# Kernel optimization log

Measured on AMD Instinct MI355X. Metric: run time of the kernel, lower is better.

The kernel has to match this reference:

```python
import jax, jax.numpy as jnp
import numpy as np

# tree structure: B trees, layer sizes per tree 2048 -> 256 -> 32 -> 1 (arities 8, 8, 32)
B = 256
N0, N1, N2, N3 = B * 2048, B * 256, B * 32, B * 1
D_IN, HID, OUT = 128, 256, 10
EPS = 1e-5


def _bn(x, g, b):
    # BatchNorm1d, training-mode batch stats (biased variance), as in torch
    mu = jnp.mean(x, axis=0)
    var = jnp.var(x, axis=0)
    return (x - mu) * jax.lax.rsqrt(var + EPS) * g + b


def _tree_layer(pooled, w1, b1, bn1g, bn1b, w2, b2, bng, bnb):
    # MLP(2 layers): Linear -> BN -> ReLU -> Linear, then outer BN -> ReLU (next_layer)
    z = jax.nn.relu(_bn(pooled @ w1 + b1, bn1g, bn1b))
    z = z @ w2 + b2
    return jax.nn.relu(_bn(z, bng, bnb))


def setup_inputs() -> dict:
    key = jax.random.key(0)
    ks = jax.random.split(key, 12)
    s = 0.05
    ar = lambda n: jnp.arange(n, dtype=jnp.int32)
    inp = {
        'x': jax.random.normal(ks[0], (N0, D_IN), jnp.float32),
        # child -> parent index (global, trees are contiguous blocks)
        'parent1': ar(N0) // 8,
        'parent2': ar(N1) // 8,
        'parent3': ar(N2) // 32,
        # node -> tree id per layer (for sum tree-pooling readout)
        'tree0': ar(N0) // 2048,
        'tree1': ar(N1) // 256,
        'tree2': ar(N2) // 32,
        # layer 1 MLP (input_dim -> hidden)
        'l1_w1': jax.random.normal(ks[1], (D_IN, HID), jnp.float32) * s,
        'l1_b1': jnp.zeros((HID,), jnp.float32),
        'l1_bn1g': jnp.ones((HID,), jnp.float32),
        'l1_bn1b': jnp.zeros((HID,), jnp.float32),
        'l1_w2': jax.random.normal(ks[2], (HID, HID), jnp.float32) * s,
        'l1_b2': jnp.zeros((HID,), jnp.float32),
        'l1_bng': jnp.ones((HID,), jnp.float32),
        'l1_bnb': jnp.zeros((HID,), jnp.float32),
        # layers 2 and 3 MLPs (hidden -> hidden), stacked on axis 0
        'lw1': jax.random.normal(ks[3], (2, HID, HID), jnp.float32) * s,
        'lb1': jnp.zeros((2, HID), jnp.float32),
        'lbn1g': jnp.ones((2, HID), jnp.float32),
        'lbn1b': jnp.zeros((2, HID), jnp.float32),
        'lw2': jax.random.normal(ks[4], (2, HID, HID), jnp.float32) * s,
        'lb2': jnp.zeros((2, HID), jnp.float32),
        'lbng': jnp.ones((2, HID), jnp.float32),
        'lbnb': jnp.zeros((2, HID), jnp.float32),
        # prediction heads
        'pred0_w': jax.random.normal(ks[5], (D_IN, OUT), jnp.float32) * s,
        'pred0_b': jnp.zeros((OUT,), jnp.float32),
        'predh_w': jax.random.normal(ks[6], (3, HID, OUT), jnp.float32) * s,
        'predh_b': jnp.zeros((3, OUT), jnp.float32),
    }
    return inp


def reference(x, parent1, parent2, parent3, tree0, tree1, tree2,
              l1_w1, l1_b1, l1_bn1g, l1_bn1b, l1_w2, l1_b2, l1_bng, l1_bnb,
              lw1, lb1, lbn1g, lbn1b, lw2, lb2, lbng, lbnb,
              pred0_w, pred0_b, predh_w, predh_b):
    seg = jax.ops.segment_sum
    h0 = x
    # layer 1: sparse child pooling (spmm == segment_sum) + MLP + BN + ReLU
    h1 = _tree_layer(seg(h0, parent1, num_segments=N1),
                     l1_w1, l1_b1, l1_bn1g, l1_bn1b, l1_w2, l1_b2, l1_bng, l1_bnb)
    h2 = _tree_layer(seg(h1, parent2, num_segments=N2),
                     lw1[0], lb1[0], lbn1g[0], lbn1b[0], lw2[0], lb2[0], lbng[0], lbnb[0])
    h3 = _tree_layer(seg(h2, parent3, num_segments=N3),
                     lw1[1], lb1[1], lbn1g[1], lbn1b[1], lw2[1], lb2[1], lbng[1], lbnb[1])
    # sum tree-pooling readout over layers 0..depth-1, plus root-layer linear
    score = seg(h0, tree0, num_segments=B) @ pred0_w + pred0_b
    score = score + seg(h1, tree1, num_segments=B) @ predh_w[0] + predh_b[0]
    score = score + seg(h2, tree2, num_segments=B) @ predh_w[1] + predh_b[1]
    score = score + h3 @ predh_w[2] + predh_b[2]  # h3 has 1 root per tree -> [B, OUT]
    return score
```

## Files before the change

### kernel.cpp

```cpp
#include <hip/hip_runtime.h>
#include <hip/hip_bf16.h>


#define N0 (256*2048)
#define N1 (256*256)
#define N2 (256*32)
#define NB 256
#define BN_EPS 1e-5f
#define NSLOT 8

typedef __attribute__((ext_vector_type(8))) __bf16 bf16x8;
typedef __attribute__((ext_vector_type(8))) unsigned short u16x8;
typedef __attribute__((ext_vector_type(4))) unsigned short u16x4;
typedef __attribute__((ext_vector_type(4))) float f32x4;

__device__ inline float bf2f(unsigned short b) {
    unsigned u = ((unsigned)b) << 16;
    float f; __builtin_memcpy(&f, &u, 4); return f;
}
__device__ inline unsigned short f2bf(float f) {
    unsigned u; __builtin_memcpy(&u, &f, 4);
    u += 0x7fff + ((u >> 16) & 1);
    return (unsigned short)(u >> 16);
}

__global__ __launch_bounds__(256) void prep_weights(const float* __restrict__ l1_w1,
                                                    const float* __restrict__ l1_w2,
                                                    const float* __restrict__ lw1,
                                                    const float* __restrict__ lw2,
                                                    unsigned short* __restrict__ Wt) {
    int idx = blockIdx.x * 256 + threadIdx.x;
    if (idx >= 360448) return;
    float v;
    if (idx < 32768) {
        int n = idx >> 7, k = idx & 127;
        v = l1_w1[k * 256 + n];
    } else if (idx < 98304) {
        int j = idx - 32768, n = j >> 8, k = j & 255;
        v = l1_w2[k * 256 + n];
    } else if (idx < 163840) {
        int j = idx - 98304, n = j >> 8, k = j & 255;
        v = lw1[k * 256 + n];
    } else if (idx < 229376) {
        int j = idx - 163840, n = j >> 8, k = j & 255;
        v = lw2[k * 256 + n];
    } else if (idx < 294912) {
        int j = idx - 229376, n = j >> 8, k = j & 255;
        v = lw1[65536 + k * 256 + n];
    } else {
        int j = idx - 294912, n = j >> 8, k = j & 255;
        v = lw2[65536 + k * 256 + n];
    }
    Wt[idx] = f2bf(v);
}

__device__ inline void bn_prologue(int tid, const float* __restrict__ partials,
                                   const float* __restrict__ g, const float* __restrict__ b,
                                   float invM, float* sc_lds, float* sh_lds) {
    if (tid < 256) {
        float s = 0.f, s2 = 0.f;
#pragma unroll
        for (int k = 0; k < NSLOT; ++k) {
            s  += partials[k * 512 + tid];
            s2 += partials[k * 512 + 256 + tid];
        }
        float mean = s * invM;
        float var = s2 * invM - mean * mean;
        float sc = g[tid] * rsqrtf(var + BN_EPS);
        sc_lds[tid] = sc;
        sh_lds[tid] = b[tid] - mean * sc;
    }
}

__global__ __launch_bounds__(256) void pool8_128(const float* __restrict__ x,
                                                 unsigned short* __restrict__ out,
                                                 float* __restrict__ ts0) {
    int tid = threadIdx.x;
    int c4 = tid & 31, pl = tid >> 5;
    int p = blockIdx.x * 8 + pl;
    int tree = blockIdx.x >> 5;
    const f32x4* xp = reinterpret_cast<const f32x4*>(x + (size_t)p * 8 * 128 + c4 * 4);
    f32x4 s = {0.f, 0.f, 0.f, 0.f};
#pragma unroll
    for (int c = 0; c < 8; ++c) s += xp[c * 32];
    u16x4 o;
#pragma unroll
    for (int e = 0; e < 4; ++e) o[e] = f2bf(s[e]);
    *reinterpret_cast<u16x4*>(out + (size_t)p * 128 + c4 * 4) = o;
    __shared__ float red[4][32][4];
    int w = tid >> 6;
    f32x4 t = s;
#pragma unroll
    for (int e = 0; e < 4; ++e) t[e] += __shfl_xor(t[e], 32);
    if ((tid & 63) < 32) {
#pragma unroll
        for (int e = 0; e < 4; ++e) red[w][c4][e] = t[e];
    }
    __syncthreads();
    if (tid < 128) {
        int cc = tid >> 2, e = tid & 3;
        float v = red[0][cc][e] + red[1][cc][e] + red[2][cc][e] + red[3][cc][e];
        atomicAdd(&ts0[tree * 128 + tid], v);
    }
}

template <int GROUP, bool TS>
__global__ __launch_bounds__(256) void pool_bn_relu(const unsigned short* __restrict__ Z,
                                                    const float* __restrict__ partials,
                                                    const float* __restrict__ g,
                                                    const float* __restrict__ b,
                                                    float invM,
                                                    unsigned short* __restrict__ out,
                                                    float* __restrict__ ts) {
    __shared__ float sc_lds[256], sh_lds[256];
    int tid = threadIdx.x;
    bn_prologue(tid, partials, g, b, invM, sc_lds, sh_lds);
    __syncthreads();
    int c8 = tid & 31, pl = tid >> 5;
    size_t p = (size_t)blockIdx.x * 8 + pl;
    int d0 = c8 * 8;
    float sc[8], sh[8], s[8];
#pragma unroll
    for (int e = 0; e < 8; ++e) { sc[e] = sc_lds[d0 + e]; sh[e] = sh_lds[d0 + e]; s[e] = 0.f; }
#pragma unroll
    for (int gi = 0; gi < GROUP; ++gi) {
        u16x8 z = *reinterpret_cast<const u16x8*>(Z + (p * GROUP + gi) * 256 + d0);
#pragma unroll
        for (int e = 0; e < 8; ++e) {
            float f = sc[e] * bf2f(z[e]) + sh[e];
            s[e] += f > 0.f ? f : 0.f;
        }
    }
    u16x8 o;
#pragma unroll
    for (int e = 0; e < 8; ++e) o[e] = f2bf(s[e]);
    *reinterpret_cast<u16x8*>(out + p * 256 + d0) = o;
    if (TS) {
        __shared__ float red[4][32][8];
        int tree = blockIdx.x >> 2;
        int w = tid >> 6;
#pragma unroll
        for (int e = 0; e < 8; ++e) s[e] += __shfl_xor(s[e], 32);
        if ((tid & 63) < 32) {
#pragma unroll
            for (int e = 0; e < 8; ++e) red[w][c8][e] = s[e];
        }
        __syncthreads();
        {
            int cc = tid >> 3, e = tid & 7;
            float v = red[0][cc][e] + red[1][cc][e] + red[2][cc][e] + red[3][cc][e];
            atomicAdd(&ts[tree * 256 + tid], v);
        }
    }
}

template <int KD, bool BN_A, int BM>
__global__ __launch_bounds__(BM * 4) void mfma_gemm(const unsigned short* __restrict__ A,
                                                    const float* __restrict__ partials_in,
                                                    const float* __restrict__ bn_g,
                                                    const float* __restrict__ bn_b,
                                                    float invM,
                                                    const unsigned short* __restrict__ Wt,
                                                    const float* __restrict__ bias,
                                                    unsigned short* __restrict__ C,
                                                    float* __restrict__ stat_partials) {
    constexpr int LDA = 72;
    constexpr int NT = BM * 4;
    __shared__ unsigned short Asb[BM * LDA];
    __shared__ unsigned short Bsb[256 * LDA];
    __shared__ float sc_lds[256], sh_lds[256];
    const int tid = threadIdx.x;
    if (BN_A) {
        bn_prologue(tid, partials_in, bn_g, bn_b, invM, sc_lds, sh_lds);
        __syncthreads();
    }
    const int m0 = blockIdx.x * BM;
    const int wave = tid >> 6, lane = tid & 63;
    const int q = lane >> 4, r = lane & 15;
    const int wc = wave & 3, wr = wave >> 2;

    f32x4 acc[4][4];
#pragma unroll
    for (int i = 0; i < 4; ++i)
#pragma unroll
        for (int j = 0; j < 4; ++j) acc[i][j] = (f32x4){0.f, 0.f, 0.f, 0.f};

    for (int k0 = 0; k0 < KD; k0 += 64) {
#pragma unroll
        for (int i = 0; i < 2; ++i) {
            int v = tid + i * NT;
            int row = v >> 3, kc = v & 7;
            u16x8 d = *reinterpret_cast<const u16x8*>(A + (size_t)(m0 + row) * KD + k0 + kc * 8);
            if (BN_A) {
                u16x8 o;
#pragma unroll
                for (int e = 0; e < 8; ++e) {
                    int k = k0 + kc * 8 + e;
                    float f = sc_lds[k] * bf2f(d[e]) + sh_lds[k];
                    o[e] = f2bf(f > 0.f ? f : 0.f);
                }
                d = o;
            }
            *reinterpret_cast<u16x8*>(&Asb[row * LDA + kc * 8]) = d;
        }
#pragma unroll
        for (int i = 0; i < 2048 / NT; ++i) {
            int v = tid + i * NT;
            int n = v >> 3, kc = v & 7;
            u16x8 d = *reinterpret_cast<const u16x8*>(Wt + (size_t)n * KD + k0 + kc * 8);
            *reinterpret_cast<u16x8*>(&Bsb[n * LDA + kc * 8]) = d;
        }
        __syncthreads();
#pragma unroll
        for (int s = 0; s < 2; ++s) {
            bf16x8 a[4], b[4];
#pragma unroll
            for (int i = 0; i < 4; ++i)
                a[i] = *reinterpret_cast<const bf16x8*>(&Asb[(wr * 64 + i * 16 + r) * LDA + s * 32 + q * 8]);
#pragma unroll
            for (int j = 0; j < 4; ++j)
                b[j] = *reinterpret_cast<const bf16x8*>(&Bsb[(wc * 64 + j * 16 + r) * LDA + s * 32 + q * 8]);
#pragma unroll
            for (int i = 0; i < 4; ++i)
#pragma unroll
                for (int j = 0; j < 4; ++j)
                    acc[i][j] = __builtin_amdgcn_mfma_f32_16x16x32_bf16(a[i], b[j], acc[i][j], 0, 0, 0);
        }
        __syncthreads();
    }

    float sj[4], s2j[4];
#pragma unroll
    for (int j = 0; j < 4; ++j) {
        float bj = bias[wc * 64 + j * 16 + r];
        float s = 0.f, s2 = 0.f;
#pragma unroll
        for (int i = 0; i < 4; ++i)
#pragma unroll
            for (int e = 0; e < 4; ++e) {
                acc[i][j][e] += bj;
                float v = acc[i][j][e];
                s += v; s2 += v * v;
            }
        s  += __shfl_xor(s, 16);  s  += __shfl_xor(s, 32);
        s2 += __shfl_xor(s2, 16); s2 += __shfl_xor(s2, 32);
        sj[j] = s; s2j[j] = s2;
    }
#pragma unroll
    for (int i = 0; i < 4; ++i)
#pragma unroll
        for (int e = 0; e < 4; ++e) {
            size_t row = m0 + wr * 64 + i * 16 + q * 4 + e;
#pragma unroll
            for (int j = 0; j < 4; ++j)
                C[row * 256 + wc * 64 + j * 16 + r] = f2bf(acc[i][j][e]);
        }
    if (q == 0) {
        int slot = blockIdx.x & (NSLOT - 1);
#pragma unroll
        for (int j = 0; j < 4; ++j) {
            int col = wc * 64 + j * 16 + r;
            atomicAdd(&stat_partials[slot * 512 + col], sj[j]);
            atomicAdd(&stat_partials[slot * 512 + 256 + col], s2j[j]);
        }
    }
}

__global__ __launch_bounds__(256) void head_kernel(const float* __restrict__ ts0,
                                                   const float* __restrict__ ts1,
                                                   const unsigned short* __restrict__ p3,
                                                   const unsigned short* __restrict__ Z3b,
                                                   const float* __restrict__ partials,
                                                   const float* __restrict__ g,
                                                   const float* __restrict__ b,
                                                   float invM,
                                                   const float* __restrict__ p0w,
                                                   const float* __restrict__ p0b,
                                                   const float* __restrict__ phw,
                                                   const float* __restrict__ phb,
                                                   float* __restrict__ out) {
    __shared__ float sc_lds[256], sh_lds[256];
    int t = blockIdx.x, d = threadIdx.x;
    bn_prologue(d, partials, g, b, invM, sc_lds, sh_lds);
    __syncthreads();
    float acc[10];
#pragma unroll
    for (int o = 0; o < 10; ++o) acc[o] = 0.f;
    if (d < 128) {
        float v = ts0[t * 128 + d];
#pragma unroll
        for (int o = 0; o < 10; ++o) acc[o] += v * p0w[d * 10 + o];
    }
    {
        float v = ts1[t * 256 + d];
#pragma unroll
        for (int o = 0; o < 10; ++o) acc[o] += v * phw[d * 10 + o];
    }
    {
        float v = bf2f(p3[t * 256 + d]);
#pragma unroll
        for (int o = 0; o < 10; ++o) acc[o] += v * phw[2560 + d * 10 + o];
    }
    {
        float v = sc_lds[d] * bf2f(Z3b[t * 256 + d]) + sh_lds[d];
        v = v > 0.f ? v : 0.f;
#pragma unroll
        for (int o = 0; o < 10; ++o) acc[o] += v * phw[5120 + d * 10 + o];
    }
    __shared__ float red[256];
    for (int o = 0; o < 10; ++o) {
        red[d] = acc[o];
        __syncthreads();
        for (int s = 128; s > 0; s >>= 1) {
            if (d < s) red[d] += red[d + s];
            __syncthreads();
        }
        if (d == 0) out[t * 10 + o] = red[0] + p0b[o] + phb[o] + phb[10 + o] + phb[20 + o];
        __syncthreads();
    }
}

extern "C" void kernel_launch(void* const* d_in, const int* in_sizes, int n_in,
                              void* d_out, int out_size, void* d_ws, size_t ws_size,
                              hipStream_t stream) {
    const float* x       = (const float*)d_in[0];
    const float* l1_w1   = (const float*)d_in[7];
    const float* l1_b1   = (const float*)d_in[8];
    const float* l1_bn1g = (const float*)d_in[9];
    const float* l1_bn1b = (const float*)d_in[10];
    const float* l1_w2   = (const float*)d_in[11];
    const float* l1_b2   = (const float*)d_in[12];
    const float* l1_bng  = (const float*)d_in[13];
    const float* l1_bnb  = (const float*)d_in[14];
    const float* lw1     = (const float*)d_in[15];
    const float* lb1     = (const float*)d_in[16];
    const float* lbn1g   = (const float*)d_in[17];
    const float* lbn1b   = (const float*)d_in[18];
    const float* lw2     = (const float*)d_in[19];
    const float* lb2     = (const float*)d_in[20];
    const float* lbng    = (const float*)d_in[21];
    const float* lbnb    = (const float*)d_in[22];
    const float* pred0_w = (const float*)d_in[23];
    const float* pred0_b = (const float*)d_in[24];
    const float* predh_w = (const float*)d_in[25];
    const float* predh_b = (const float*)d_in[26];
    float* out = (float*)d_out;

    uint8_t* wsb = (uint8_t*)d_ws;
    unsigned short* pooled1 = (unsigned short*)(wsb);
    unsigned short* Z1      = (unsigned short*)(wsb + (16ull << 20));
    unsigned short* Z2      = (unsigned short*)(wsb + (48ull << 20));
    unsigned short* pooled2 = (unsigned short*)(wsb + (80ull << 20));
    unsigned short* Z2a     = (unsigned short*)(wsb + (84ull << 20));
    unsigned short* Z2b     = (unsigned short*)(wsb + (88ull << 20));
    unsigned short* pooled3 = (unsigned short*)(wsb + (92ull << 20));
    unsigned short* Z3a     = (unsigned short*)(wsb + (92ull << 20) + 131072);
    unsigned short* Z3b     = (unsigned short*)(wsb + (92ull << 20) + 262144);
    unsigned short* Wt      = (unsigned short*)(wsb + (93ull << 20));
    float* zbase = (float*)(wsb + (94ull << 20));
    float* ts0   = zbase;
    float* ts1   = zbase + 32768;
    float* stats = zbase + 32768 + 65536;
    auto SP = [&](int i) { return stats + i * (NSLOT * 512); };
    size_t zbytes = (32768 + 65536 + 6 * NSLOT * 512) * sizeof(float);

    hipMemsetAsync(zbase, 0, zbytes, stream);
    prep_weights<<<1408, 256, 0, stream>>>(l1_w1, l1_w2, lw1, lw2, Wt);

    pool8_128<<<N1 / 8, 256, 0, stream>>>(x, pooled1, ts0);
    mfma_gemm<128, false, 128><<<N1 / 128, 512, 0, stream>>>(
        pooled1, nullptr, nullptr, nullptr, 0.f, Wt, l1_b1, Z1, SP(0));
    mfma_gemm<256, true, 128><<<N1 / 128, 512, 0, stream>>>(
        Z1, SP(0), l1_bn1g, l1_bn1b, 1.f / N1, Wt + 32768, l1_b2, Z2, SP(1));
    pool_bn_relu<8, true><<<N2 / 8, 256, 0, stream>>>(
        Z2, SP(1), l1_bng, l1_bnb, 1.f / N1, pooled2, ts1);

    mfma_gemm<256, false, 64><<<N2 / 64, 256, 0, stream>>>(
        pooled2, nullptr, nullptr, nullptr, 0.f, Wt + 98304, lb1, Z2a, SP(2));
    mfma_gemm<256, true, 64><<<N2 / 64, 256, 0, stream>>>(
        Z2a, SP(2), lbn1g, lbn1b, 1.f / N2, Wt + 163840, lb2, Z2b, SP(3));
    pool_bn_relu<32, false><<<NB / 8, 256, 0, stream>>>(
        Z2b, SP(3), lbng, lbnb, 1.f / N2, pooled3, nullptr);

    mfma_gemm<256, false, 64><<<NB / 64, 256, 0, stream>>>(
        pooled3, nullptr, nullptr, nullptr, 0.f, Wt + 229376, lb1 + 256, Z3a, SP(4));
    mfma_gemm<256, true, 64><<<NB / 64, 256, 0, stream>>>(
        Z3a, SP(4), lbn1g + 256, lbn1b + 256, 1.f / NB, Wt + 294912, lb2 + 256, Z3b, SP(5));

    head_kernel<<<NB, 256, 0, stream>>>(ts0, ts1, pooled3, Z3b, SP(5),
                                        lbng + 256, lbnb + 256, 1.f / NB,
                                        pred0_w, pred0_b, predh_w, predh_b, out);
}
```

Measured before the change: 196.9 us.

## Fuse child pooling into the following GEMMs for layers one and two

The pooling of x (sum of 8 children) now happens inside the first GEMM kernel, which writes pooled rows straight to LDS instead of a global buffer. Likewise the BN+ReLU+pool of Z2 is folded into the layer-2 first GEMM, with the tree-sum readout atomics done in the same pass. This removes two kernel launches and the global write/read of pooled1 and pooled2. In exchange, each GEMM block does more serial load work before its MFMAs, the per-thread tree-sum atomics are less reduced (more atomics), and LDS use grows.

```diff
diff --git a/kernel.cpp b/kernel.cpp
--- a/kernel.cpp
+++ b/kernel.cpp
@@ -72,84 +72,225 @@
     }
 }
 
-__global__ __launch_bounds__(256) void pool8_128(const float* __restrict__ x,
-                                                 unsigned short* __restrict__ out,
-                                                 float* __restrict__ ts0) {
-    int tid = threadIdx.x;
-    int c4 = tid & 31, pl = tid >> 5;
-    int p = blockIdx.x * 8 + pl;
-    int tree = blockIdx.x >> 5;
-    const f32x4* xp = reinterpret_cast<const f32x4*>(x + (size_t)p * 8 * 128 + c4 * 4);
-    f32x4 s = {0.f, 0.f, 0.f, 0.f};
-#pragma unroll
-    for (int c = 0; c < 8; ++c) s += xp[c * 32];
-    u16x4 o;
-#pragma unroll
-    for (int e = 0; e < 4; ++e) o[e] = f2bf(s[e]);
-    *reinterpret_cast<u16x4*>(out + (size_t)p * 128 + c4 * 4) = o;
-    __shared__ float red[4][32][4];
-    int w = tid >> 6;
-    f32x4 t = s;
-#pragma unroll
-    for (int e = 0; e < 4; ++e) t[e] += __shfl_xor(t[e], 32);
-    if ((tid & 63) < 32) {
-#pragma unroll
-        for (int e = 0; e < 4; ++e) red[w][c4][e] = t[e];
-    }
+__global__ __launch_bounds__(512) void gemm1_fused(const float* __restrict__ x,
+                                                   const unsigned short* __restrict__ Wt,
+                                                   const float* __restrict__ bias,
+                                                   unsigned short* __restrict__ Z1,
+                                                   float* __restrict__ stat_partials,
+                                                   float* __restrict__ ts0) {
+    constexpr int LDA = 136, LDB = 72;
+    __shared__ unsigned short Asb[128 * LDA];
+    __shared__ unsigned short Bsb[256 * LDB];
+    const int tid = threadIdx.x;
+    const int c4 = tid & 31, rg = tid >> 5;
+    const int m0 = blockIdx.x * 128;
+    const int tree = blockIdx.x >> 1;
+    f32x4 colp = {0.f, 0.f, 0.f, 0.f};
+#pragma unroll
+    for (int i = 0; i < 8; ++i) {
+        int row = rg * 8 + i;
+        const f32x4* xp = reinterpret_cast<const f32x4*>(x + (size_t)(m0 + row) * 1024 + c4 * 4);
+        f32x4 s = {0.f, 0.f, 0.f, 0.f};
+#pragma unroll
+        for (int c = 0; c < 8; ++c) s += xp[c * 32];
+        u16x4 o;
+#pragma unroll
+        for (int e = 0; e < 4; ++e) o[e] = f2bf(s[e]);
+        *reinterpret_cast<u16x4*>(&Asb[row * LDA + c4 * 4]) = o;
+        colp += s;
+    }
+#pragma unroll
+    for (int e = 0; e < 4; ++e) atomicAdd(&ts0[tree * 128 + c4 * 4 + e], colp[e]);
+
+    const int wave = tid >> 6, lane = tid & 63;
+    const int q = lane >> 4, r = lane & 15;
+    const int wc = wave & 3, wr = wave >> 2;
+    f32x4 acc[4][4];
+#pragma unroll
+    for (int i = 0; i < 4; ++i)
+#pragma unroll
+        for (int j = 0; j < 4; ++j) acc[i][j] = (f32x4){0.f, 0.f, 0.f, 0.f};
+
+#pragma unroll
+    for (int s2 = 0; s2 < 2; ++s2) {
+#pragma unroll
+        for (int i = 0; i < 4; ++i) {
+            int v = tid + i * 512;
+            int n = v >> 3, kc = v & 7;
+            u16x8 d = *reinterpret_cast<const u16x8*>(Wt + (size_t)n * 128 + s2 * 64 + kc * 8);
+            *reinterpret_cast<u16x8*>(&Bsb[n * LDB + kc * 8]) = d;
+        }
+        __syncthreads();
+#pragma unroll
+        for (int s = 0; s < 2; ++s) {
+            bf16x8 a[4], b[4];
+#pragma unroll
+            for (int i = 0; i < 4; ++i)
+                a[i] = *reinterpret_cast<const bf16x8*>(&Asb[(wr * 64 + i * 16 + r) * LDA + s2 * 64 + s * 32 + q * 8]);
+#pragma unroll
+            for (int j = 0; j < 4; ++j)
+                b[j] = *reinterpret_cast<const bf16x8*>(&Bsb[(wc * 64 + j * 16 + r) * LDB + s * 32 + q * 8]);
+#pragma unroll
+            for (int i = 0; i < 4; ++i)
+#pragma unroll
+                for (int j = 0; j < 4; ++j)
+                    acc[i][j] = __builtin_amdgcn_mfma_f32_16x16x32_bf16(a[i], b[j], acc[i][j], 0, 0, 0);
+        }
+        __syncthreads();
+    }
+    float sj[4], s2j[4];
+#pragma unroll
+    for (int j = 0; j < 4; ++j) {
+        float bj = bias[wc * 64 + j * 16 + r];
+        float s = 0.f, s2 = 0.f;
+#pragma unroll
+        for (int i = 0; i < 4; ++i)
+#pragma unroll
+            for (int e = 0; e < 4; ++e) {
+                acc[i][j][e] += bj;
+                float v = acc[i][j][e];
+                s += v; s2 += v * v;
+            }
+        s  += __shfl_xor(s, 16);  s  += __shfl_xor(s, 32);
+        s2 += __shfl_xor(s2, 16); s2 += __shfl_xor(s2, 32);
+        sj[j] = s; s2j[j] = s2;
+    }
+#pragma unroll
+    for (int i = 0; i < 4; ++i)
+#pragma unroll
+        for (int e = 0; e < 4; ++e) {
+            size_t row = m0 + wr * 64 + i * 16 + q * 4 + e;
+#pragma unroll
+            for (int j = 0; j < 4; ++j)
+                Z1[row * 256 + wc * 64 + j * 16 + r] = f2bf(acc[i][j][e]);
+        }
+    if (q == 0) {
+        int slot = blockIdx.x & (NSLOT - 1);
+#pragma unroll
+        for (int j = 0; j < 4; ++j) {
+            int col = wc * 64 + j * 16 + r;
+            atomicAdd(&stat_partials[slot * 512 + col], sj[j]);
+            atomicAdd(&stat_partials[slot * 512 + 256 + col], s2j[j]);
+        }
+    }
+}
+
+__global__ __launch_bounds__(256) void gemm2_fused(const unsigned short* __restrict__ Z2,
+                                                   const float* __restrict__ partials_in,
+                                                   const float* __restrict__ bn_g,
+                                                   const float* __restrict__ bn_b,
+                                                   float invM,
+                                                   const unsigned short* __restrict__ Wt2,
+                                                   const float* __restrict__ bias,
+                                                   unsigned short* __restrict__ Z2a,
+                                                   float* __restrict__ stat_partials,
+                                                   float* __restrict__ ts1) {
+    constexpr int LDA = 264, LDB = 72;
+    __shared__ unsigned short Asb[64 * LDA];
+    __shared__ unsigned short Bsb[256 * LDB];
+    __shared__ float sc_lds[256], sh_lds[256];
+    const int tid = threadIdx.x;
+    bn_prologue(tid, partials_in, bn_g, bn_b, invM, sc_lds, sh_lds);
     __syncthreads();
-    if (tid < 128) {
-        int cc = tid >> 2, e = tid & 3;
-        float v = red[0][cc][e] + red[1][cc][e] + red[2][cc][e] + red[3][cc][e];
-        atomicAdd(&ts0[tree * 128 + tid], v);
-    }
-}
-
-template <int GROUP, bool TS>
-__global__ __launch_bounds__(256) void pool_bn_relu(const unsigned short* __restrict__ Z,
-                                                    const float* __restrict__ partials,
-                                                    const float* __restrict__ g,
-                                                    const float* __restrict__ b,
-                                                    float invM,
-                                                    unsigned short* __restrict__ out,
-                                                    float* __restrict__ ts) {
-    __shared__ float sc_lds[256], sh_lds[256];
-    int tid = threadIdx.x;
-    bn_prologue(tid, partials, g, b, invM, sc_lds, sh_lds);
-    __syncthreads();
-    int c8 = tid & 31, pl = tid >> 5;
-    size_t p = (size_t)blockIdx.x * 8 + pl;
-    int d0 = c8 * 8;
-    float sc[8], sh[8], s[8];
-#pragma unroll
-    for (int e = 0; e < 8; ++e) { sc[e] = sc_lds[d0 + e]; sh[e] = sh_lds[d0 + e]; s[e] = 0.f; }
-#pragma unroll
-    for (int gi = 0; gi < GROUP; ++gi) {
-        u16x8 z = *reinterpret_cast<const u16x8*>(Z + (p * GROUP + gi) * 256 + d0);
-#pragma unroll
-        for (int e = 0; e < 8; ++e) {
-            float f = sc[e] * bf2f(z[e]) + sh[e];
-            s[e] += f > 0.f ? f : 0.f;
-        }
-    }
-    u16x8 o;
-#pragma unroll
-    for (int e = 0; e < 8; ++e) o[e] = f2bf(s[e]);
-    *reinterpret_cast<u16x8*>(out + p * 256 + d0) = o;
-    if (TS) {
-        __shared__ float red[4][32][8];
-        int tree = blockIdx.x >> 2;
-        int w = tid >> 6;
-#pragma unroll
-        for (int e = 0; e < 8; ++e) s[e] += __shfl_xor(s[e], 32);
-        if ((tid & 63) < 32) {
-#pragma unroll
-            for (int e = 0; e < 8; ++e) red[w][c8][e] = s[e];
-        }
-        __syncthreads();
-        {
-            int cc = tid >> 3, e = tid & 7;
-            float v = red[0][cc][e] + red[1][cc][e] + red[2][cc][e] + red[3][cc][e];
-            atomicAdd(&ts[tree * 256 + tid], v);
+    const int c8 = tid & 31, rg = tid >> 5;
+    const int m0 = blockIdx.x * 64;
+    const int d0 = c8 * 8;
+    float sc[8], sh[8], colp[8];
+#pragma unroll
+    for (int e = 0; e < 8; ++e) { sc[e] = sc_lds[d0 + e]; sh[e] = sh_lds[d0 + e]; colp[e] = 0.f; }
+#pragma unroll
+    for (int i = 0; i < 8; ++i) {
+        int row = rg * 8 + i;
+        float s[8];
+#pragma unroll
+        for (int e = 0; e < 8; ++e) s[e] = 0.f;
+#pragma unroll
+        for (int c = 0; c < 8; ++c) {
+            u16x8 z = *reinterpret_cast<const u16x8*>(Z2 + ((size_t)(m0 + row) * 8 + c) * 256 + d0);
+#pragma unroll
+            for (int e = 0; e < 8; ++e) {
+                float f = sc[e] * bf2f(z[e]) + sh[e];
+                s[e] += f > 0.f ? f : 0.f;
+            }
+        }
+        u16x8 o;
+#pragma unroll
+        for (int e = 0; e < 8; ++e) { o[e] = f2bf(s[e]); colp[e] += s[e]; }
+        *reinterpret_cast<u16x8*>(&Asb[row * LDA + d0]) = o;
+    }
+    {
+        int tree = blockIdx.x * 2 + (rg >> 2);
+#pragma unroll
+        for (int e = 0; e < 8; ++e) atomicAdd(&ts1[tree * 256 + d0 + e], colp[e]);
+    }
+    const int wave = tid >> 6, lane = tid & 63;
+    const int q = lane >> 4, r = lane & 15;
+    const int wc = wave;
+    f32x4 acc[4][4];
+#pragma unroll
+    for (int i = 0; i < 4; ++i)
+#pragma unroll
+        for (int j = 0; j < 4; ++j) acc[i][j] = (f32x4){0.f, 0.f, 0.f, 0.f};
+
+    for (int kt = 0; kt < 4; ++kt) {
+#pragma unroll
+        for (int i = 0; i < 8; ++i) {
+            int v = tid + i * 256;
+            int n = v >> 3, kc = v & 7;
+            u16x8 d = *reinterpret_cast<const u16x8*>(Wt2 + (size_t)n * 256 + kt * 64 + kc * 8);
+            *reinterpret_cast<u16x8*>(&Bsb[n * LDB + kc * 8]) = d;
+        }
+        __syncthreads();
+#pragma unroll
+        for (int s = 0; s < 2; ++s) {
+            bf16x8 a[4], b[4];
+#pragma unroll
+            for (int i = 0; i < 4; ++i)
+                a[i] = *reinterpret_cast<const bf16x8*>(&Asb[(i * 16 + r) * LDA + kt * 64 + s * 32 + q * 8]);
+#pragma unroll
+            for (int j = 0; j < 4; ++j)
+                b[j] = *reinterpret_cast<const bf16x8*>(&Bsb[(wc * 64 + j * 16 + r) * LDB + s * 32 + q * 8]);
+#pragma unroll
+            for (int i = 0; i < 4; ++i)
+#pragma unroll
+                for (int j = 0; j < 4; ++j)
+                    acc[i][j] = __builtin_amdgcn_mfma_f32_16x16x32_bf16(a[i], b[j], acc[i][j], 0, 0, 0);
+        }
+        __syncthreads();
+    }
+    float sj[4], s2j[4];
+#pragma unroll
+    for (int j = 0; j < 4; ++j) {
+        float bj = bias[wc * 64 + j * 16 + r];
+        float s = 0.f, s2 = 0.f;
+#pragma unroll
+        for (int i = 0; i < 4; ++i)
+#pragma unroll
+            for (int e = 0; e < 4; ++e) {
+                acc[i][j][e] += bj;
+                float v = acc[i][j][e];
+                s += v; s2 += v * v;
+            }
+        s  += __shfl_xor(s, 16);  s  += __shfl_xor(s, 32);
+        s2 += __shfl_xor(s2, 16); s2 += __shfl_xor(s2, 32);
+        sj[j] = s; s2j[j] = s2;
+    }
+#pragma unroll
+    for (int i = 0; i < 4; ++i)
+#pragma unroll
+        for (int e = 0; e < 4; ++e) {
+            size_t row = m0 + i * 16 + q * 4 + e;
+#pragma unroll
+            for (int j = 0; j < 4; ++j)
+                Z2a[row * 256 + wc * 64 + j * 16 + r] = f2bf(acc[i][j][e]);
+        }
+    if (q == 0) {
+        int slot = blockIdx.x & (NSLOT - 1);
+#pragma unroll
+        for (int j = 0; j < 4; ++j) {
+            int col = wc * 64 + j * 16 + r;
+            atomicAdd(&stat_partials[slot * 512 + col], sj[j]);
+            atomicAdd(&stat_partials[slot * 512 + 256 + col], s2j[j]);
         }
     }
 }
@@ -228,7 +369,6 @@
         }
         __syncthreads();
     }
-
     float sj[4], s2j[4];
 #pragma unroll
     for (int j = 0; j < 4; ++j) {
@@ -264,6 +404,37 @@
             atomicAdd(&stat_partials[slot * 512 + 256 + col], s2j[j]);
         }
     }
+}
+
+__global__ __launch_bounds__(256) void pool_bn_relu32(const unsigned short* __restrict__ Z,
+                                                      const float* __restrict__ partials,
+                                                      const float* __restrict__ g,
+                                                      const float* __restrict__ b,
+                                                      float invM,
+                                                      unsigned short* __restrict__ out) {
+    __shared__ float sc_lds[256], sh_lds[256];
+    int tid = threadIdx.x;
+    bn_prologue(tid, partials, g, b, invM, sc_lds, sh_lds);
+    __syncthreads();
+    int c8 = tid & 31, pl = tid >> 5;
+    size_t p = (size_t)blockIdx.x * 8 + pl;
+    int d0 = c8 * 8;
+    float sc[8], sh[8], s[8];
+#pragma unroll
+    for (int e = 0; e < 8; ++e) { sc[e] = sc_lds[d0 + e]; sh[e] = sh_lds[d0 + e]; s[e] = 0.f; }
+#pragma unroll
+    for (int gi = 0; gi < 32; ++gi) {
+        u16x8 z = *reinterpret_cast<const u16x8*>(Z + (p * 32 + gi) * 256 + d0);
+#pragma unroll
+        for (int e = 0; e < 8; ++e) {
+            float f = sc[e] * bf2f(z[e]) + sh[e];
+            s[e] += f > 0.f ? f : 0.f;
+        }
+    }
+    u16x8 o;
+#pragma unroll
+    for (int e = 0; e < 8; ++e) o[e] = f2bf(s[e]);
+    *reinterpret_cast<u16x8*>(out + p * 256 + d0) = o;
 }
 
 __global__ __launch_bounds__(256) void head_kernel(const float* __restrict__ ts0,
@@ -347,10 +518,8 @@
     float* out = (float*)d_out;
 
     uint8_t* wsb = (uint8_t*)d_ws;
-    unsigned short* pooled1 = (unsigned short*)(wsb);
     unsigned short* Z1      = (unsigned short*)(wsb + (16ull << 20));
     unsigned short* Z2      = (unsigned short*)(wsb + (48ull << 20));
-    unsigned short* pooled2 = (unsigned short*)(wsb + (80ull << 20));
     unsigned short* Z2a     = (unsigned short*)(wsb + (84ull << 20));
     unsigned short* Z2b     = (unsigned short*)(wsb + (88ull << 20));
     unsigned short* pooled3 = (unsigned short*)(wsb + (92ull << 20));
@@ -367,20 +536,15 @@
     hipMemsetAsync(zbase, 0, zbytes, stream);
     prep_weights<<<1408, 256, 0, stream>>>(l1_w1, l1_w2, lw1, lw2, Wt);
 
-    pool8_128<<<N1 / 8, 256, 0, stream>>>(x, pooled1, ts0);
-    mfma_gemm<128, false, 128><<<N1 / 128, 512, 0, stream>>>(
-        pooled1, nullptr, nullptr, nullptr, 0.f, Wt, l1_b1, Z1, SP(0));
+    gemm1_fused<<<N1 / 128, 512, 0, stream>>>(x, Wt, l1_b1, Z1, SP(0), ts0);
     mfma_gemm<256, true, 128><<<N1 / 128, 512, 0, stream>>>(
         Z1, SP(0), l1_bn1g, l1_bn1b, 1.f / N1, Wt + 32768, l1_b2, Z2, SP(1));
-    pool_bn_relu<8, true><<<N2 / 8, 256, 0, stream>>>(
-        Z2, SP(1), l1_bng, l1_bnb, 1.f / N1, pooled2, ts1);
-
-    mfma_gemm<256, false, 64><<<N2 / 64, 256, 0, stream>>>(
-        pooled2, nullptr, nullptr, nullptr, 0.f, Wt + 98304, lb1, Z2a, SP(2));
+
+    gemm2_fused<<<N2 / 64, 256, 0, stream>>>(
+        Z2, SP(1), l1_bng, l1_bnb, 1.f / N1, Wt + 98304, lb1, Z2a, SP(2), ts1);
     mfma_gemm<256, true, 64><<<N2 / 64, 256, 0, stream>>>(
         Z2a, SP(2), lbn1g, lbn1b, 1.f / N2, Wt + 163840, lb2, Z2b, SP(3));
-    pool_bn_relu<32, false><<<NB / 8, 256, 0, stream>>>(
-        Z2b, SP(3), lbng, lbnb, 1.f / N2, pooled3, nullptr);
+    pool_bn_relu32<<<NB / 8, 256, 0, stream>>>(Z2b, SP(3), lbng, lbnb, 1.f / N2, pooled3);
 
     mfma_gemm<256, false, 64><<<NB / 64, 256, 0, stream>>>(
         pooled3, nullptr, nullptr, nullptr, 0.f, Wt + 229376, lb1 + 256, Z3a, SP(4));
```

New measurement: 191.4 us. -2.8%, faster.
